# Kernel tuning notes

Hardware: AMD Instinct MI355X
Metric: run time of the kernel (lower is better)

Reference implementation:

```python
import jax, jax.numpy as jnp
import numpy as np

B, IN_CH, OUT_CH = 4, 64, 128
N_HIGH, N_LOW = 163842, 40962
GROUPS, EPS, SLOPE = 4, 1e-5, 0.2


def setup_inputs() -> dict:
    key = jax.random.key(0)
    ks = jax.random.split(key, 6)
    x = jax.random.normal(ks[0], (B, IN_CH, N_HIGH), jnp.float32)
    pool_neigh = jax.random.randint(ks[1], (N_LOW * 7,), 0, N_HIGH, dtype=jnp.int32)
    conv_neigh = jax.random.randint(ks[2], (N_LOW * 7,), 0, N_LOW, dtype=jnp.int32)
    W1 = jax.random.normal(ks[3], (OUT_CH, 7 * IN_CH), jnp.float32) / np.float32(np.sqrt(7 * IN_CH))
    b1 = jnp.zeros((OUT_CH,), jnp.float32)
    W2 = jax.random.normal(ks[4], (OUT_CH, 7 * OUT_CH), jnp.float32) / np.float32(np.sqrt(7 * OUT_CH))
    b2 = jnp.zeros((OUT_CH,), jnp.float32)
    return dict(x=x, pool_neigh=pool_neigh, conv_neigh=conv_neigh,
                W1=W1, b1=b1, gn1_w=jnp.ones((OUT_CH,), jnp.float32), gn1_b=jnp.zeros((OUT_CH,), jnp.float32),
                W2=W2, b2=b2, gn2_w=jnp.ones((OUT_CH,), jnp.float32), gn2_b=jnp.zeros((OUT_CH,), jnp.float32))


def _mean_pool(x, pool_neigh):
    # x: (B, C, N_high); pool_neigh: (N_low*7,) -> (B, C, N_low)
    g = x[:, :, pool_neigh].reshape(x.shape[0], x.shape[1], -1, 7)
    return g.mean(axis=-1)


def _onering_conv(x, neigh, W, b):
    # x: (B, C, N); neigh: (N*7,); W: (O, 7*C). Torch Linear over gathered
    # (N*7, C).view(N, 7*C): neighbor-major, channel-minor concatenation.
    Bb, C, N = x.shape
    feat = x[:, :, neigh].reshape(Bb, C, N, 7)            # (B, C, N, 7)
    feat = jnp.transpose(feat, (0, 2, 3, 1)).reshape(Bb, N, 7 * C)  # (B, N, 7C)
    out = jnp.einsum('bnf,of->bno', feat, W) + b          # (B, N, O)
    return jnp.transpose(out, (0, 2, 1))                  # (B, O, N)


def _group_norm(x, w, b):
    # x: (B, C, N), normalize per (group, sample) over (C//G, N)
    Bb, C, N = x.shape
    xg = x.reshape(Bb, GROUPS, C // GROUPS, N)
    mu = xg.mean(axis=(2, 3), keepdims=True)
    var = ((xg - mu) ** 2).mean(axis=(2, 3), keepdims=True)
    xn = ((xg - mu) * jax.lax.rsqrt(var + EPS)).reshape(Bb, C, N)
    return xn * w[None, :, None] + b[None, :, None]


def _leaky_relu(x):
    return jnp.where(x >= 0, x, SLOPE * x)


def reference(x, pool_neigh, conv_neigh, W1, b1, gn1_w, gn1_b, W2, b2, gn2_w, gn2_b):
    h = _mean_pool(x, pool_neigh)
    h = _leaky_relu(_group_norm(_onering_conv(h, conv_neigh, W1, b1), gn1_w, gn1_b))
    h = _leaky_relu(_group_norm(_onering_conv(h, conv_neigh, W2, b2), gn2_w, gn2_b))
    return h
```

## Files before the change

### kernel.cpp

```cpp
#include <hip/hip_runtime.h>

#define B_SZ 4
#define IN_CH 64
#define OUT_CH 128
#define NHI 163842
#define NLO 40962
#define EPS_GN 1e-5f
#define SLOPE 0.2f

typedef __attribute__((ext_vector_type(8))) short short8;
typedef __attribute__((ext_vector_type(16))) float f32x16;

__device__ inline ushort f2bf(float f) {
    union { float f; unsigned u; } v; v.f = f;
    unsigned r = v.u + 0x7FFF + ((v.u >> 16) & 1);
    return (ushort)(r >> 16);
}
__device__ inline float bf2f(ushort h) {
    union { unsigned u; float f; } v; v.u = ((unsigned)h) << 16;
    return v.f;
}

__global__ void k_transpose_x(const float* __restrict__ x, ushort* __restrict__ xT) {
    __shared__ float t[64][65];
    const int b   = blockIdx.y;
    const int n0  = blockIdx.x * 64;
    const int tid = threadIdx.x;
    const int nq  = tid & 15;
    const int c0  = tid >> 4;
    const bool full = (n0 + 64) <= NHI;
    if (full) {
#pragma unroll
        for (int r = 0; r < 4; ++r) {
            int c = c0 + r * 16;
            float4 v = *(const float4*)&x[((long)b * IN_CH + c) * NHI + n0 + nq * 4];
            t[c][nq * 4 + 0] = v.x; t[c][nq * 4 + 1] = v.y;
            t[c][nq * 4 + 2] = v.z; t[c][nq * 4 + 3] = v.w;
        }
    } else {
        for (int r = 0; r < 4; ++r) {
            int c = c0 + r * 16;
            for (int e = 0; e < 4; ++e) {
                int n = n0 + nq * 4 + e;
                t[c][nq * 4 + e] = (n < NHI) ? x[((long)b * IN_CH + c) * NHI + n] : 0.f;
            }
        }
    }
    __syncthreads();
    const int n  = tid >> 2;
    const int cc = (tid & 3) * 16;
    if (n0 + n < NHI) {
        short8 o0, o1;
#pragma unroll
        for (int e = 0; e < 8; ++e) {
            o0[e] = (short)f2bf(t[cc + e][n]);
            o1[e] = (short)f2bf(t[cc + 8 + e][n]);
        }
        ushort* p = &xT[((long)b * NHI + n0 + n) * 64 + cc];
        *(short8*)p = o0;
        *(short8*)(p + 8) = o1;
    }
}

__global__ void k_prep_w(const float* __restrict__ W, ushort* __restrict__ Wb, int K) {
    int i = blockIdx.x * 256 + threadIdx.x;
    if (i >= K * 128) return;
    int k = i / 128, o = i % 128;
    int kg = k >> 3, e = k & 7;
    Wb[(((long)kg * 128 + o) * 8) + e] = f2bf(W[(long)o * K + k]);
}

__global__ void k_pool(const ushort* __restrict__ xT, const int* __restrict__ pn,
                       ushort* __restrict__ h1) {
    long t = (long)blockIdx.x * 256 + threadIdx.x;
    const long total = (long)B_SZ * NLO * 8;
    if (t >= total) return;
    int  cq = (int)(t & 7);
    long bn = t >> 3;
    int  n  = (int)(bn % NLO);
    int  b  = (int)(bn / NLO);
    float acc[8] = {};
#pragma unroll
    for (int j = 0; j < 7; ++j) {
        int idx = pn[n * 7 + j];
        short8 v = *(const short8*)&xT[((long)b * NHI + idx) * 64 + cq * 8];
#pragma unroll
        for (int e = 0; e < 8; ++e) acc[e] += bf2f((ushort)v[e]);
    }
    short8 o;
#pragma unroll
    for (int e = 0; e < 8; ++e) o[e] = (short)f2bf(acc[e] * (1.f / 7.f));
    *(short8*)&h1[bn * 64 + cq * 8] = o;
}

__device__ inline int aidx(int kg, int nn) {
    return (kg * 64 + (nn ^ ((kg & 7) << 1))) * 8;
}

template <int CIN>
__global__ __launch_bounds__(256, 4)
void k_conv_mfma(const ushort* __restrict__ src, const int* __restrict__ nbr,
                 const ushort* __restrict__ Wb, const float* __restrict__ bias,
                 ushort* __restrict__ out, float* __restrict__ part) {
    constexpr int KG = CIN / 8;
    constexpr int CT = CIN / 32;
    __shared__ ushort Asm[2][KG * 64 * 8];
    __shared__ float  red[4][2][2];

    const int b     = blockIdx.y;
    const int n0    = blockIdx.x * 64;
    const int tid   = threadIdx.x;
    const int lane  = tid & 63;
    const int wave  = tid >> 6;
    const int wr    = wave >> 1, wc = wave & 1;
    const int l31   = lane & 31;
    const int khalf = lane >> 5;

    const int s_nn = tid >> 2;
    const int s_kq = tid & 3;
    const int r0 = min(n0 + s_nn, NLO - 1);
    int nb[7];
#pragma unroll
    for (int j = 0; j < 7; ++j) nb[j] = nbr[r0 * 7 + j];

    const long srcb = (long)b * NLO * CIN;
    f32x16 acc[2] = {};
    short8 aH[CT], aL[CT];

    {
        const ushort* p = &src[srcb + (long)nb[0] * CIN + s_kq * 8];
        short8 t[CT];
#pragma unroll
        for (int i = 0; i < CT; ++i) t[i] = *(const short8*)(p + i * 32);
#pragma unroll
        for (int i = 0; i < CT; ++i)
            *(short8*)&Asm[0][aidx(s_kq + 4 * i, s_nn)] = t[i];
        const ushort* p1 = &src[srcb + (long)nb[1] * CIN + s_kq * 8];
#pragma unroll
        for (int i = 0; i < CT; ++i) aH[i] = *(const short8*)(p1 + i * 32);
    }
    __syncthreads();

#pragma unroll
    for (int j = 0; j < 7; ++j) {
        const int cur = j & 1;
        if (j + 2 < 7) {
            const ushort* p = &src[srcb + (long)nb[j + 2] * CIN + s_kq * 8];
#pragma unroll
            for (int i = 0; i < CT; ++i) aL[i] = *(const short8*)(p + i * 32);
        }
        if (j + 1 < 7) {
#pragma unroll
            for (int i = 0; i < CT; ++i)
                *(short8*)&Asm[cur ^ 1][aidx(s_kq + 4 * i, s_nn)] = aH[i];
        }
        const ushort* wbj = &Wb[((long)j * KG * 128 + wc * 64 + l31) * 8];
#pragma unroll
        for (int kh = 0; kh < KG / 2; ++kh) {
            const int kg = 2 * kh + khalf;
            short8 A0 = *(const short8*)&Asm[cur][aidx(kg, wr * 32 + l31)];
            short8 B0 = *(const short8*)(wbj + (long)kg * 128 * 8);
            short8 B1 = *(const short8*)(wbj + (long)kg * 128 * 8 + 32 * 8);
            acc[0] = __builtin_amdgcn_mfma_f32_32x32x16_bf16(A0, B0, acc[0], 0, 0, 0);
            acc[1] = __builtin_amdgcn_mfma_f32_32x32x16_bf16(A0, B1, acc[1], 0, 0, 0);
        }
#pragma unroll
        for (int i = 0; i < CT; ++i) aH[i] = aL[i];
        __syncthreads();
    }

    float bia[2];
#pragma unroll
    for (int n = 0; n < 2; ++n) bia[n] = bias[wc * 64 + n * 32 + l31];
    float s[2] = {}, q[2] = {};
#pragma unroll
    for (int n = 0; n < 2; ++n)
#pragma unroll
        for (int r = 0; r < 16; ++r) {
            int crow = (r & 3) + 8 * (r >> 2) + 4 * khalf;
            int row  = n0 + wr * 32 + crow;
            float v  = acc[n][r] + bia[n];
            if (row < NLO) {
                out[((long)b * NLO + row) * 128 + wc * 64 + n * 32 + l31] = f2bf(v);
                s[n] += v; q[n] += v * v;
            }
        }
#pragma unroll
    for (int n = 0; n < 2; ++n)
#pragma unroll
        for (int off = 32; off > 0; off >>= 1) {
            s[n] += __shfl_down(s[n], off);
            q[n] += __shfl_down(q[n], off);
        }
    if (lane == 0) {
#pragma unroll
        for (int n = 0; n < 2; ++n) { red[wave][n][0] = s[n]; red[wave][n][1] = q[n]; }
    }
    __syncthreads();
    if (tid < 8) {
        int g = tid >> 1, isq = tid & 1;
        int gwc = g >> 1, gn = g & 1;
        float v = red[gwc][gn][isq] + red[2 + gwc][gn][isq];
        part[(((long)b * gridDim.x + blockIdx.x) * 4 + g) * 2 + isq] = v;
    }
}

__global__ void k_finalize(const float* __restrict__ part, int nblk,
                           const float* __restrict__ w, const float* __restrict__ bb,
                           float* __restrict__ scale, float* __restrict__ shift) {
    const int b = blockIdx.x >> 2, g = blockIdx.x & 3;
    const int tid = threadIdx.x;
    float s = 0.f, ss = 0.f;
    for (int k = tid; k < nblk; k += 256) {
        s  += part[(((long)b * nblk + k) * 4 + g) * 2 + 0];
        ss += part[(((long)b * nblk + k) * 4 + g) * 2 + 1];
    }
#pragma unroll
    for (int off = 32; off > 0; off >>= 1) {
        s += __shfl_down(s, off); ss += __shfl_down(ss, off);
    }
    __shared__ float red[8];
    __shared__ float fin[2];
    const int wave = tid >> 6, lane = tid & 63;
    if (lane == 0) { red[wave * 2] = s; red[wave * 2 + 1] = ss; }
    __syncthreads();
    if (tid == 0) {
        float as = red[0] + red[2] + red[4] + red[6];
        float aq = red[1] + red[3] + red[5] + red[7];
        const float cnt = 32.f * NLO;
        float mu  = as / cnt;
        float var = aq / cnt - mu * mu;
        fin[0] = mu; fin[1] = rsqrtf(var + EPS_GN);
    }
    __syncthreads();
    if (tid < 32) {
        int c = g * 32 + tid;
        float sc = fin[1] * w[c];
        scale[b * 128 + c] = sc;
        shift[b * 128 + c] = bb[c] - fin[0] * sc;
    }
}

__global__ void k_gnapply(const ushort* __restrict__ y, const float* __restrict__ sc,
                          const float* __restrict__ sh, ushort* __restrict__ yp) {
    long t = (long)blockIdx.x * 256 + threadIdx.x;
    const long total = (long)B_SZ * NLO * 16;
    if (t >= total) return;
    int  c8 = (int)(t & 15);
    long bn = t >> 4;
    int  b  = (int)(bn / NLO);
    short8 v = *(const short8*)&y[bn * 128 + c8 * 8];
    short8 o;
#pragma unroll
    for (int e = 0; e < 8; ++e) {
        int c = c8 * 8 + e;
        float f = bf2f((ushort)v[e]) * sc[b * 128 + c] + sh[b * 128 + c];
        f = fmaxf(f, SLOPE * f);
        o[e] = (short)f2bf(f);
    }
    *(short8*)&yp[bn * 128 + c8 * 8] = o;
}

__global__ void k_output(const ushort* __restrict__ y2, const float* __restrict__ scale,
                         const float* __restrict__ shift, float* __restrict__ out) {
    __shared__ float t[32][129];
    const int b   = blockIdx.y;
    const int n0  = blockIdx.x * 32;
    const int tid = threadIdx.x;
    const float* scb = &scale[b * 128];
    const float* shb = &shift[b * 128];
    const int c8 = (tid & 15) * 8;
#pragma unroll
    for (int r = 0; r < 2; ++r) {
        int nn = (tid >> 4) + r * 16;
        int n  = n0 + nn;
        if (n < NLO) {
            short8 v = *(const short8*)&y2[((long)b * NLO + n) * 128 + c8];
#pragma unroll
            for (int e = 0; e < 8; ++e) {
                int c = c8 + e;
                float f = bf2f((ushort)v[e]) * scb[c] + shb[c];
                t[nn][c] = fmaxf(f, SLOPE * f);
            }
        } else {
#pragma unroll
            for (int e = 0; e < 8; ++e) t[nn][c8 + e] = 0.f;
        }
    }
    __syncthreads();
    const int n4 = (tid & 7) * 4;
    const bool full = (n0 + 32) <= NLO;
#pragma unroll
    for (int r = 0; r < 4; ++r) {
        int c = (tid >> 3) + r * 32;
        long o = ((long)b * 128 + c) * NLO + n0 + n4;
        if (full) {
            float2 v0 = make_float2(t[n4][c], t[n4 + 1][c]);
            float2 v1 = make_float2(t[n4 + 2][c], t[n4 + 3][c]);
            *(float2*)&out[o]     = v0;
            *(float2*)&out[o + 2] = v1;
        } else {
            for (int e = 0; e < 4; ++e)
                if (n0 + n4 + e < NLO) out[o + e] = t[n4 + e][c];
        }
    }
}

extern "C" void kernel_launch(void* const* d_in, const int* in_sizes, int n_in,
                              void* d_out, int out_size, void* d_ws, size_t ws_size,
                              hipStream_t stream) {
    const float* x   = (const float*)d_in[0];
    const int*   pn  = (const int*)d_in[1];
    const int*   cn  = (const int*)d_in[2];
    const float* W1  = (const float*)d_in[3];
    const float* b1  = (const float*)d_in[4];
    const float* g1w = (const float*)d_in[5];
    const float* g1b = (const float*)d_in[6];
    const float* W2  = (const float*)d_in[7];
    const float* b2  = (const float*)d_in[8];
    const float* g2w = (const float*)d_in[9];
    const float* g2b = (const float*)d_in[10];
    float* out = (float*)d_out;
    char*  base = (char*)d_ws;

    ushort* xT  = (ushort*)(base + 0);
    ushort* y1  = (ushort*)(base + 0);
    ushort* y1p = (ushort*)(base + 44000000);
    ushort* h1  = (ushort*)(base + 88000000);
    ushort* y2  = (ushort*)(base + 110000000);
    ushort* wb1 = (ushort*)(base + 152000000);
    ushort* wb2 = (ushort*)(base + 152200000);
    float*  p1  = (float*)(base + 152500000);
    float*  p2  = (float*)(base + 152600000);
    float*  sc1 = (float*)(base + 152700000);
    float*  sh1 = sc1 + 512;
    float*  sc2 = (float*)(base + 152710000);
    float*  sh2 = sc2 + 512;

    const int NBLK = (NLO + 63) / 64;

    k_transpose_x<<<dim3((NHI + 63) / 64, B_SZ), 256, 0, stream>>>(x, xT);
    k_prep_w<<<(448 * 128 + 255) / 256, 256, 0, stream>>>(W1, wb1, 448);
    k_prep_w<<<(896 * 128 + 255) / 256, 256, 0, stream>>>(W2, wb2, 896);
    k_pool<<<(int)(((long)B_SZ * NLO * 8 + 255) / 256), 256, 0, stream>>>(xT, pn, h1);
    k_conv_mfma<64><<<dim3(NBLK, B_SZ), 256, 0, stream>>>(h1, cn, wb1, b1, y1, p1);
    k_finalize<<<16, 256, 0, stream>>>(p1, NBLK, g1w, g1b, sc1, sh1);
    k_gnapply<<<(int)(((long)B_SZ * NLO * 16 + 255) / 256), 256, 0, stream>>>(y1, sc1, sh1, y1p);
    k_conv_mfma<128><<<dim3(NBLK, B_SZ), 256, 0, stream>>>(y1p, cn, wb2, b2, y2, p2);
    k_finalize<<<16, 256, 0, stream>>>(p2, NBLK, g2w, g2b, sc2, sh2);
    k_output<<<dim3((NLO + 31) / 32, B_SZ), 256, 0, stream>>>(y2, sc2, sh2, out);
}
```

Measured before the change: 258.9 us.

## Restructure one-ring conv as single-wave blocks loading gathered rows directly into registers

Each conv block becomes a single 64-lane wave that handles 32 vertices across all 128 output channels. The gathered neighbor features now load straight from global memory into MFMA A-operand registers with double buffering, so the shared-memory staging and block-wide barriers are gone. Each wave now reads the full weight matrix per tile, which doubles weight traffic per output, and smaller tiles mean more blocks and more partial-sum records. The partial-stats buffers move to workspace regions that are dead at that point.

```diff
diff --git a/kernel.cpp b/kernel.cpp
--- a/kernel.cpp
+++ b/kernel.cpp
@@ -93,115 +93,83 @@
     *(short8*)&h1[bn * 64 + cq * 8] = o;
 }
 
-__device__ inline int aidx(int kg, int nn) {
-    return (kg * 64 + (nn ^ ((kg & 7) << 1))) * 8;
-}
-
 template <int CIN>
-__global__ __launch_bounds__(256, 4)
+__global__ __launch_bounds__(64, 2)
 void k_conv_mfma(const ushort* __restrict__ src, const int* __restrict__ nbr,
                  const ushort* __restrict__ Wb, const float* __restrict__ bias,
                  ushort* __restrict__ out, float* __restrict__ part) {
-    constexpr int KG = CIN / 8;
-    constexpr int CT = CIN / 32;
-    __shared__ ushort Asm[2][KG * 64 * 8];
-    __shared__ float  red[4][2][2];
-
+    constexpr int KH = CIN / 16;
     const int b     = blockIdx.y;
-    const int n0    = blockIdx.x * 64;
-    const int tid   = threadIdx.x;
-    const int lane  = tid & 63;
-    const int wave  = tid >> 6;
-    const int wr    = wave >> 1, wc = wave & 1;
+    const int n0    = blockIdx.x * 32;
+    const int lane  = threadIdx.x;
     const int l31   = lane & 31;
     const int khalf = lane >> 5;
 
-    const int s_nn = tid >> 2;
-    const int s_kq = tid & 3;
-    const int r0 = min(n0 + s_nn, NLO - 1);
+    const int row = min(n0 + l31, NLO - 1);
     int nb[7];
 #pragma unroll
-    for (int j = 0; j < 7; ++j) nb[j] = nbr[r0 * 7 + j];
+    for (int j = 0; j < 7; ++j) nb[j] = nbr[row * 7 + j];
 
     const long srcb = (long)b * NLO * CIN;
-    f32x16 acc[2] = {};
-    short8 aH[CT], aL[CT];
+    const int  koff = khalf * 8;
+
+    f32x16 acc[4] = {};
+    short8 abuf[2][KH];
 
     {
-        const ushort* p = &src[srcb + (long)nb[0] * CIN + s_kq * 8];
-        short8 t[CT];
-#pragma unroll
-        for (int i = 0; i < CT; ++i) t[i] = *(const short8*)(p + i * 32);
-#pragma unroll
-        for (int i = 0; i < CT; ++i)
-            *(short8*)&Asm[0][aidx(s_kq + 4 * i, s_nn)] = t[i];
-        const ushort* p1 = &src[srcb + (long)nb[1] * CIN + s_kq * 8];
-#pragma unroll
-        for (int i = 0; i < CT; ++i) aH[i] = *(const short8*)(p1 + i * 32);
-    }
-    __syncthreads();
+        const ushort* p = &src[srcb + (long)nb[0] * CIN + koff];
+#pragma unroll
+        for (int kh = 0; kh < KH; ++kh) abuf[0][kh] = *(const short8*)(p + kh * 16);
+    }
 
 #pragma unroll
     for (int j = 0; j < 7; ++j) {
-        const int cur = j & 1;
-        if (j + 2 < 7) {
-            const ushort* p = &src[srcb + (long)nb[j + 2] * CIN + s_kq * 8];
-#pragma unroll
-            for (int i = 0; i < CT; ++i) aL[i] = *(const short8*)(p + i * 32);
-        }
+        const ushort* wj = &Wb[(((long)j * 2 * KH + khalf) * 128 + l31) * 8];
+#pragma unroll
+        for (int kh = 0; kh < KH; ++kh) {
+            const ushort* wk = wj + (long)(2 * kh) * 128 * 8;
+#pragma unroll
+            for (int nt = 0; nt < 4; ++nt) {
+                short8 bf = *(const short8*)(wk + nt * 32 * 8);
+                acc[nt] = __builtin_amdgcn_mfma_f32_32x32x16_bf16(abuf[j & 1][kh], bf, acc[nt], 0, 0, 0);
+            }
+        }
+        __builtin_amdgcn_sched_barrier(0);
         if (j + 1 < 7) {
-#pragma unroll
-            for (int i = 0; i < CT; ++i)
-                *(short8*)&Asm[cur ^ 1][aidx(s_kq + 4 * i, s_nn)] = aH[i];
-        }
-        const ushort* wbj = &Wb[((long)j * KG * 128 + wc * 64 + l31) * 8];
-#pragma unroll
-        for (int kh = 0; kh < KG / 2; ++kh) {
-            const int kg = 2 * kh + khalf;
-            short8 A0 = *(const short8*)&Asm[cur][aidx(kg, wr * 32 + l31)];
-            short8 B0 = *(const short8*)(wbj + (long)kg * 128 * 8);
-            short8 B1 = *(const short8*)(wbj + (long)kg * 128 * 8 + 32 * 8);
-            acc[0] = __builtin_amdgcn_mfma_f32_32x32x16_bf16(A0, B0, acc[0], 0, 0, 0);
-            acc[1] = __builtin_amdgcn_mfma_f32_32x32x16_bf16(A0, B1, acc[1], 0, 0, 0);
-        }
-#pragma unroll
-        for (int i = 0; i < CT; ++i) aH[i] = aL[i];
-        __syncthreads();
-    }
-
-    float bia[2];
-#pragma unroll
-    for (int n = 0; n < 2; ++n) bia[n] = bias[wc * 64 + n * 32 + l31];
-    float s[2] = {}, q[2] = {};
-#pragma unroll
-    for (int n = 0; n < 2; ++n)
+            const ushort* p = &src[srcb + (long)nb[j + 1] * CIN + koff];
+#pragma unroll
+            for (int kh = 0; kh < KH; ++kh)
+                abuf[(j + 1) & 1][kh] = *(const short8*)(p + kh * 16);
+        }
+        __builtin_amdgcn_sched_barrier(0);
+    }
+
+    float s[4] = {}, q[4] = {};
+#pragma unroll
+    for (int nt = 0; nt < 4; ++nt) {
+        const float bia = bias[nt * 32 + l31];
 #pragma unroll
         for (int r = 0; r < 16; ++r) {
             int crow = (r & 3) + 8 * (r >> 2) + 4 * khalf;
-            int row  = n0 + wr * 32 + crow;
-            float v  = acc[n][r] + bia[n];
-            if (row < NLO) {
-                out[((long)b * NLO + row) * 128 + wc * 64 + n * 32 + l31] = f2bf(v);
-                s[n] += v; q[n] += v * v;
+            int orow = n0 + crow;
+            float v  = acc[nt][r] + bia;
+            if (orow < NLO) {
+                out[((long)b * NLO + orow) * 128 + nt * 32 + l31] = f2bf(v);
+                s[nt] += v; q[nt] += v * v;
             }
         }
-#pragma unroll
-    for (int n = 0; n < 2; ++n)
+    }
+#pragma unroll
+    for (int nt = 0; nt < 4; ++nt)
 #pragma unroll
         for (int off = 32; off > 0; off >>= 1) {
-            s[n] += __shfl_down(s[n], off);
-            q[n] += __shfl_down(q[n], off);
+            s[nt] += __shfl_down(s[nt], off);
+            q[nt] += __shfl_down(q[nt], off);
         }
     if (lane == 0) {
-#pragma unroll
-        for (int n = 0; n < 2; ++n) { red[wave][n][0] = s[n]; red[wave][n][1] = q[n]; }
-    }
-    __syncthreads();
-    if (tid < 8) {
-        int g = tid >> 1, isq = tid & 1;
-        int gwc = g >> 1, gn = g & 1;
-        float v = red[gwc][gn][isq] + red[2 + gwc][gn][isq];
-        part[(((long)b * gridDim.x + blockIdx.x) * 4 + g) * 2 + isq] = v;
+        float* pp = &part[((long)b * gridDim.x + blockIdx.x) * 8];
+#pragma unroll
+        for (int g = 0; g < 4; ++g) { pp[g * 2] = s[g]; pp[g * 2 + 1] = q[g]; }
     }
 }
 
@@ -212,8 +180,8 @@
     const int tid = threadIdx.x;
     float s = 0.f, ss = 0.f;
     for (int k = tid; k < nblk; k += 256) {
-        s  += part[(((long)b * nblk + k) * 4 + g) * 2 + 0];
-        ss += part[(((long)b * nblk + k) * 4 + g) * 2 + 1];
+        s  += part[((long)b * nblk + k) * 8 + g * 2 + 0];
+        ss += part[((long)b * nblk + k) * 8 + g * 2 + 1];
     }
 #pragma unroll
     for (int off = 32; off > 0; off >>= 1) {
@@ -330,23 +298,23 @@
     ushort* y2  = (ushort*)(base + 110000000);
     ushort* wb1 = (ushort*)(base + 152000000);
     ushort* wb2 = (ushort*)(base + 152200000);
-    float*  p1  = (float*)(base + 152500000);
-    float*  p2  = (float*)(base + 152600000);
+    float*  p1  = (float*)(base + 110000000);
+    float*  p2  = (float*)(base + 88000000);
     float*  sc1 = (float*)(base + 152700000);
     float*  sh1 = sc1 + 512;
     float*  sc2 = (float*)(base + 152710000);
     float*  sh2 = sc2 + 512;
 
-    const int NBLK = (NLO + 63) / 64;
+    const int NBLK = (NLO + 31) / 32;
 
     k_transpose_x<<<dim3((NHI + 63) / 64, B_SZ), 256, 0, stream>>>(x, xT);
     k_prep_w<<<(448 * 128 + 255) / 256, 256, 0, stream>>>(W1, wb1, 448);
     k_prep_w<<<(896 * 128 + 255) / 256, 256, 0, stream>>>(W2, wb2, 896);
     k_pool<<<(int)(((long)B_SZ * NLO * 8 + 255) / 256), 256, 0, stream>>>(xT, pn, h1);
-    k_conv_mfma<64><<<dim3(NBLK, B_SZ), 256, 0, stream>>>(h1, cn, wb1, b1, y1, p1);
+    k_conv_mfma<64><<<dim3(NBLK, B_SZ), 64, 0, stream>>>(h1, cn, wb1, b1, y1, p1);
     k_finalize<<<16, 256, 0, stream>>>(p1, NBLK, g1w, g1b, sc1, sh1);
     k_gnapply<<<(int)(((long)B_SZ * NLO * 16 + 255) / 256), 256, 0, stream>>>(y1, sc1, sh1, y1p);
-    k_conv_mfma<128><<<dim3(NBLK, B_SZ), 256, 0, stream>>>(y1p, cn, wb2, b2, y2, p2);
+    k_conv_mfma<128><<<dim3(NBLK, B_SZ), 64, 0, stream>>>(y1p, cn, wb2, b2, y2, p2);
     k_finalize<<<16, 256, 0, stream>>>(p2, NBLK, g2w, g2b, sc2, sh2);
     k_output<<<dim3((NLO + 31) / 32, B_SZ), 256, 0, stream>>>(y2, sc2, sh2, out);
 }
```

Result: slower. 311.0 us (+20.2%).
